# Kernel optimization log

Measured on AMD Instinct MI355X. Metric: run time of the kernel, lower is better.

## Reference

```python
import jax, jax.numpy as jnp
import numpy as np

BLUR_SIGMA = 5.0      # init kwarg blur_sigma
N_SIGMAS_PER_SIDE = 4 # fixed in module source
FLOW_AMP = 1.0        # init kwarg flow_amp
N_DIMS = 2            # len(img_shape) - 1


def _gaussian_kernel_2d(sigma, n_sigmas_per_side):
    # separable 2D gaussian spanning n_sigmas_per_side sigmas on each side, sum-normalized
    r = int(round(n_sigmas_per_side * sigma))
    x = np.arange(-r, r + 1, dtype=np.float32)
    g = np.exp(-(x ** 2) / (2.0 * sigma ** 2))
    k = np.outer(g, g)
    k /= k.sum()
    return jnp.asarray(k, dtype=jnp.float32)  # [kh, kw] = [41, 41] for sigma=5


def setup_inputs() -> dict:
    key = jax.random.key(0)
    k1, k2 = jax.random.split(key)
    inputs = jax.random.normal(k1, (16, 512, 512, 1), dtype=jnp.float32)
    # uniform in [0,1); scaled to [-flow_amp, flow_amp) inside reference
    rand_noise = jax.random.uniform(k2, (16, 512, 512, 2), dtype=jnp.float32)
    return {"inputs": inputs, "rand_noise": rand_noise}


def reference(inputs, rand_noise):
    # kernel tiled identically over the n_dims flow channels (depthwise, multiplier=1)
    k2d = _gaussian_kernel_2d(BLUR_SIGMA, N_SIGMAS_PER_SIDE)
    kernel = jnp.tile(k2d[:, :, None, None], (1, 1, 1, N_DIMS))  # HWIO: [41,41,1,2]
    # K.random_uniform(minval=-flow_amp, maxval=flow_amp)
    flow = rand_noise * (2.0 * FLOW_AMP) - FLOW_AMP  # [B,H,W,2]
    # tf.nn.depthwise_conv2d(..., strides=1, padding='SAME')
    out = jax.lax.conv_general_dilated(
        flow, kernel,
        window_strides=(1, 1),
        padding="SAME",
        dimension_numbers=("NHWC", "HWIO", "NHWC"),
        feature_group_count=N_DIMS,
    )  # [B,H,W,2] == reshape to (-1,)+flow_shape (no-op here)
    return out
```

## Files before the change

### kernel.cpp

```cpp
#include <hip/hip_runtime.h>

#define NB   16
#define H    512
#define W    512
#define KW   41
#define HALO 20

#define TX   88
#define TY   32
#define IN_W 128
#define PVV  16
#define PX   11
#define MSTR 129
#define OSTR 89
#define SMEM_F2 (TY * MSTR)

constexpr float G[KW] = {
  0.0003354626f, 0.0007318024f, 0.0015338104f, 0.0030887172f,
  0.0059760229f, 0.0111089965f, 0.0198410947f, 0.0340474548f,
  0.0561347628f, 0.0889216176f, 0.1353352832f, 0.1978986990f,
  0.2780373005f, 0.3753110988f, 0.4867522560f, 0.6065306597f,
  0.7261490371f, 0.8352702114f, 0.9231163464f, 0.9801986733f,
  1.0f,
  0.9801986733f, 0.9231163464f, 0.8352702114f, 0.7261490371f,
  0.6065306597f, 0.4867522560f, 0.3753110988f, 0.2780373005f,
  0.1978986990f, 0.1353352832f, 0.0889216176f, 0.0561347628f,
  0.0340474548f, 0.0198410947f, 0.0111089965f, 0.0059760229f,
  0.0030887172f, 0.0015338104f, 0.0007318024f, 0.0003354626f
};

constexpr float gsum() { float s = 0.f; for (int i = 0; i < KW; ++i) s += G[i]; return s; }
constexpr float INV_S2 = 1.0f / (gsum() * gsum());

__global__ __launch_bounds__(256, 4)
void randflow_blur_kernel(const float* __restrict__ noise, float* __restrict__ out) {
    __shared__ float2 smem[SMEM_F2];

    const int tid = threadIdx.x;
    const int bx  = blockIdx.x;
    const int tx0 = bx * TX;
    const int ty0 = blockIdx.y * TY;
    const int b   = blockIdx.z;
    const float* __restrict__ src = noise + (size_t)b * (H * W * 2);

    {
        const int sx  = tid & 127;
        const int yg  = tid >> 7;
        const int gx  = tx0 + sx - HALO;
        const int cgx = min(max(gx, 0), W - 1);
        const float sa = (gx == cgx) ? 2.0f : 0.0f;
        const float sb = (gx == cgx) ? -1.0f : 0.0f;
        const int  ysb = ty0 + yg * PVV - HALO;
        const float* __restrict__ colp = src + 2 * cgx;

        float2 acc[PVV];
        #pragma unroll
        for (int p = 0; p < PVV; ++p) acc[p] = make_float2(0.f, 0.f);

        #pragma unroll
        for (int j = 0; j < PVV + KW - 1; ++j) {
            const int ys = ysb + j;
            const int cy = min(max(ys, 0), H - 1);
            const float a  = (ys == cy) ? sa : 0.0f;
            const float bb = (ys == cy) ? sb : 0.0f;
            const float2 u = *(const float2*)(colp + (size_t)cy * (W * 2));
            float2 v;
            v.x = __builtin_fmaf(u.x, a, bb);
            v.y = __builtin_fmaf(u.y, a, bb);
            #pragma unroll
            for (int p = 0; p < PVV; ++p) {
                const int t = j - p;
                if (t >= 0 && t < KW) {
                    acc[p].x = __builtin_fmaf(G[t], v.x, acc[p].x);
                    acc[p].y = __builtin_fmaf(G[t], v.y, acc[p].y);
                }
            }
        }
        #pragma unroll
        for (int p = 0; p < PVV; ++p)
            smem[(yg * PVV + p) * MSTR + sx] = acc[p];
    }
    __syncthreads();

    const int y  = tid & 31;
    const int xg = tid >> 5;
    const int x0 = xg * PX;
    float2 facc[PX];
    {
        #pragma unroll
        for (int p = 0; p < PX; ++p) facc[p] = make_float2(0.f, 0.f);
        #pragma unroll
        for (int j = 0; j < PX + KW - 1; ++j) {
            const float2 v = smem[y * MSTR + x0 + j];
            #pragma unroll
            for (int p = 0; p < PX; ++p) {
                const int t = j - p;
                if (t >= 0 && t < KW) {
                    facc[p].x = __builtin_fmaf(G[t], v.x, facc[p].x);
                    facc[p].y = __builtin_fmaf(G[t], v.y, facc[p].y);
                }
            }
        }
    }
    __syncthreads();

    #pragma unroll
    for (int p = 0; p < PX; ++p) {
        float2 r;
        r.x = facc[p].x * INV_S2;
        r.y = facc[p].y * INV_S2;
        smem[y * OSTR + x0 + p] = r;
    }
    __syncthreads();

    #pragma unroll
    for (int p = 0; p < PX; ++p) {
        const int flat = p * 256 + tid;
        const int ry = flat / TX;
        const int rx = flat - ry * TX;
        const int xo = tx0 + rx;
        if (xo < W) {
            const int yo = ty0 + ry;
            *(float2*)(out + (((size_t)b * H + yo) * W + xo) * 2) = smem[ry * OSTR + rx];
        }
    }
}

extern "C" void kernel_launch(void* const* d_in, const int* in_sizes, int n_in,
                              void* d_out, int out_size, void* d_ws, size_t ws_size,
                              hipStream_t stream) {
    const float* noise = (const float*)d_in[1];
    float* out = (float*)d_out;

    dim3 grid((W + TX - 1) / TX, H / TY, NB);
    dim3 block(256);
    randflow_blur_kernel<<<grid, block, 0, stream>>>(noise, out);
}
```

Before: 124.2 us.

## Split blur into vertical and horizontal kernels with fp16 intermediate in workspace

Replaces the fused tile kernel with two passes when workspace is large enough. The first pass does the vertical 41-tap blur straight from global memory with no halo recompute in x and stores the result as half2. The second pass does the horizontal blur from an LDS tile with a padded layout and writes float4. The split removes the fused kernel's horizontal halo redundancy, at the cost of an extra global round trip through an fp16 buffer that loses precision. The original fused kernel is kept as a fallback.

```diff
diff --git a/kernel.cpp b/kernel.cpp
--- a/kernel.cpp
+++ b/kernel.cpp
@@ -1,4 +1,5 @@
 #include <hip/hip_runtime.h>
+#include <hip/hip_fp16.h>
 
 #define NB   16
 #define H    512
@@ -6,14 +7,14 @@
 #define KW   41
 #define HALO 20
 
-#define TX   88
-#define TY   32
-#define IN_W 128
-#define PVV  16
-#define PX   11
-#define MSTR 129
-#define OSTR 89
-#define SMEM_F2 (TY * MSTR)
+#define PVV  32
+
+#define ROWS 8
+#define TLOG 552
+#define TPHYS 825
+#define PX   16
+
+__device__ __forceinline__ int PHYS(int x) { return x + ((x >> 4) << 3); }
 
 constexpr float G[KW] = {
   0.0003354626f, 0.0007318024f, 0.0015338104f, 0.0030887172f,
@@ -28,21 +29,123 @@
   0.0340474548f, 0.0198410947f, 0.0111089965f, 0.0059760229f,
   0.0030887172f, 0.0015338104f, 0.0007318024f, 0.0003354626f
 };
-
 constexpr float gsum() { float s = 0.f; for (int i = 0; i < KW; ++i) s += G[i]; return s; }
+constexpr float INV_S  = 1.0f / gsum();
 constexpr float INV_S2 = 1.0f / (gsum() * gsum());
 
-__global__ __launch_bounds__(256, 4)
-void randflow_blur_kernel(const float* __restrict__ noise, float* __restrict__ out) {
-    __shared__ float2 smem[SMEM_F2];
-
+__global__ __launch_bounds__(256, 2)
+void kv_vertical(const float* __restrict__ noise, __half2* __restrict__ mid) {
     const int tid = threadIdx.x;
     const int bx  = blockIdx.x;
-    const int tx0 = bx * TX;
-    const int ty0 = blockIdx.y * TY;
+    const int b   = blockIdx.y;
+    const int x   = (bx & 1) * 256 + tid;
+    const int yg  = bx >> 1;
+    const int ysb = yg * PVV - HALO;
+    const float* __restrict__ colp = noise + ((size_t)b * (H * W) + x) * 2;
+
+    float2 acc[PVV];
+    #pragma unroll
+    for (int p = 0; p < PVV; ++p) acc[p] = make_float2(0.f, 0.f);
+
+    #pragma unroll
+    for (int j = 0; j < PVV + KW - 1; ++j) {
+        const int ys = ysb + j;
+        const int cy = min(max(ys, 0), H - 1);
+        const float a  = (ys == cy) ? 2.0f : 0.0f;
+        const float bb = (ys == cy) ? -1.0f : 0.0f;
+        const float2 u = *(const float2*)(colp + (size_t)cy * (W * 2));
+        float2 v;
+        v.x = __builtin_fmaf(u.x, a, bb);
+        v.y = __builtin_fmaf(u.y, a, bb);
+        #pragma unroll
+        for (int p = 0; p < PVV; ++p) {
+            const int t = j - p;
+            if (t >= 0 && t < KW) {
+                acc[p].x = __builtin_fmaf(G[t], v.x, acc[p].x);
+                acc[p].y = __builtin_fmaf(G[t], v.y, acc[p].y);
+            }
+        }
+    }
+    __half2* __restrict__ mb = mid + (size_t)b * (H * W) + x;
+    #pragma unroll
+    for (int p = 0; p < PVV; ++p) {
+        float2 r;
+        r.x = acc[p].x * INV_S;
+        r.y = acc[p].y * INV_S;
+        mb[(size_t)(yg * PVV + p) * W] = __float22half2_rn(r);
+    }
+}
+
+__global__ __launch_bounds__(256, 4)
+void kh_horizontal(const __half2* __restrict__ mid, float* __restrict__ out) {
+    __shared__ __half2 tile[ROWS * TPHYS];
+
+    const int tid = threadIdx.x;
+    const int rb  = blockIdx.x;
+    const int b   = blockIdx.y;
+    const int y0  = rb * ROWS;
+    const __half2* __restrict__ mb = mid + (size_t)b * (H * W) + (size_t)y0 * W;
+
+    for (int i = tid; i < ROWS * TLOG; i += 256) {
+        const int r  = i / TLOG;
+        const int cc = i - r * TLOG;
+        const int xs = cc - HALO;
+        __half2 v = __float2half2_rn(0.0f);
+        if ((unsigned)xs < (unsigned)W) v = mb[r * W + xs];
+        tile[r * TPHYS + PHYS(cc)] = v;
+    }
+    __syncthreads();
+
+    const int y  = tid & 7;
+    const int xg = tid >> 3;
+    const int x0 = xg * PX;
+    float2 acc[PX];
+    #pragma unroll
+    for (int p = 0; p < PX; ++p) acc[p] = make_float2(0.f, 0.f);
+
+    const __half2* __restrict__ trow = tile + y * TPHYS;
+    #pragma unroll
+    for (int j = 0; j < PX + KW - 1; ++j) {
+        const float2 v = __half22float2(trow[PHYS(x0 + j)]);
+        #pragma unroll
+        for (int p = 0; p < PX; ++p) {
+            const int t = j - p;
+            if (t >= 0 && t < KW) {
+                acc[p].x = __builtin_fmaf(G[t], v.x, acc[p].x);
+                acc[p].y = __builtin_fmaf(G[t], v.y, acc[p].y);
+            }
+        }
+    }
+
+    float2* __restrict__ orow = (float2*)out + ((size_t)b * H + y0 + y) * W;
+    #pragma unroll
+    for (int q = 0; q < PX / 2; ++q) {
+        float4 r;
+        r.x = acc[2*q].x   * INV_S;
+        r.y = acc[2*q].y   * INV_S;
+        r.z = acc[2*q+1].x * INV_S;
+        r.w = acc[2*q+1].y * INV_S;
+        *(float4*)&orow[x0 + 2*q] = r;
+    }
+}
+
+#define TXF   88
+#define TYF   32
+#define PVVF  16
+#define PXF   11
+#define MSTR  129
+#define OSTR  89
+#define SMEM_F2 (TYF * MSTR)
+
+__global__ __launch_bounds__(256, 4)
+void randflow_fused(const float* __restrict__ noise, float* __restrict__ out) {
+    __shared__ float2 smem[SMEM_F2];
+    const int tid = threadIdx.x;
+    const int bx  = blockIdx.x;
+    const int tx0 = bx * TXF;
+    const int ty0 = blockIdx.y * TYF;
     const int b   = blockIdx.z;
     const float* __restrict__ src = noise + (size_t)b * (H * W * 2);
-
     {
         const int sx  = tid & 127;
         const int yg  = tid >> 7;
@@ -50,15 +153,13 @@
         const int cgx = min(max(gx, 0), W - 1);
         const float sa = (gx == cgx) ? 2.0f : 0.0f;
         const float sb = (gx == cgx) ? -1.0f : 0.0f;
-        const int  ysb = ty0 + yg * PVV - HALO;
+        const int  ysb = ty0 + yg * PVVF - HALO;
         const float* __restrict__ colp = src + 2 * cgx;
-
-        float2 acc[PVV];
-        #pragma unroll
-        for (int p = 0; p < PVV; ++p) acc[p] = make_float2(0.f, 0.f);
-
-        #pragma unroll
-        for (int j = 0; j < PVV + KW - 1; ++j) {
+        float2 acc[PVVF];
+        #pragma unroll
+        for (int p = 0; p < PVVF; ++p) acc[p] = make_float2(0.f, 0.f);
+        #pragma unroll
+        for (int j = 0; j < PVVF + KW - 1; ++j) {
             const int ys = ysb + j;
             const int cy = min(max(ys, 0), H - 1);
             const float a  = (ys == cy) ? sa : 0.0f;
@@ -68,7 +169,7 @@
             v.x = __builtin_fmaf(u.x, a, bb);
             v.y = __builtin_fmaf(u.y, a, bb);
             #pragma unroll
-            for (int p = 0; p < PVV; ++p) {
+            for (int p = 0; p < PVVF; ++p) {
                 const int t = j - p;
                 if (t >= 0 && t < KW) {
                     acc[p].x = __builtin_fmaf(G[t], v.x, acc[p].x);
@@ -77,23 +178,22 @@
             }
         }
         #pragma unroll
-        for (int p = 0; p < PVV; ++p)
-            smem[(yg * PVV + p) * MSTR + sx] = acc[p];
-    }
-    __syncthreads();
-
+        for (int p = 0; p < PVVF; ++p)
+            smem[(yg * PVVF + p) * MSTR + sx] = acc[p];
+    }
+    __syncthreads();
     const int y  = tid & 31;
     const int xg = tid >> 5;
-    const int x0 = xg * PX;
-    float2 facc[PX];
+    const int x0 = xg * PXF;
+    float2 facc[PXF];
     {
         #pragma unroll
-        for (int p = 0; p < PX; ++p) facc[p] = make_float2(0.f, 0.f);
-        #pragma unroll
-        for (int j = 0; j < PX + KW - 1; ++j) {
+        for (int p = 0; p < PXF; ++p) facc[p] = make_float2(0.f, 0.f);
+        #pragma unroll
+        for (int j = 0; j < PXF + KW - 1; ++j) {
             const float2 v = smem[y * MSTR + x0 + j];
             #pragma unroll
-            for (int p = 0; p < PX; ++p) {
+            for (int p = 0; p < PXF; ++p) {
                 const int t = j - p;
                 if (t >= 0 && t < KW) {
                     facc[p].x = __builtin_fmaf(G[t], v.x, facc[p].x);
@@ -103,21 +203,19 @@
         }
     }
     __syncthreads();
-
-    #pragma unroll
-    for (int p = 0; p < PX; ++p) {
+    #pragma unroll
+    for (int p = 0; p < PXF; ++p) {
         float2 r;
         r.x = facc[p].x * INV_S2;
         r.y = facc[p].y * INV_S2;
         smem[y * OSTR + x0 + p] = r;
     }
     __syncthreads();
-
-    #pragma unroll
-    for (int p = 0; p < PX; ++p) {
+    #pragma unroll
+    for (int p = 0; p < PXF; ++p) {
         const int flat = p * 256 + tid;
-        const int ry = flat / TX;
-        const int rx = flat - ry * TX;
+        const int ry = flat / TXF;
+        const int rx = flat - ry * TXF;
         const int xo = tx0 + rx;
         if (xo < W) {
             const int yo = ty0 + ry;
@@ -132,7 +230,15 @@
     const float* noise = (const float*)d_in[1];
     float* out = (float*)d_out;
 
-    dim3 grid((W + TX - 1) / TX, H / TY, NB);
-    dim3 block(256);
-    randflow_blur_kernel<<<grid, block, 0, stream>>>(noise, out);
-}
+    const size_t mid_bytes = (size_t)NB * H * W * sizeof(__half2);
+    if (ws_size >= mid_bytes) {
+        __half2* mid = (__half2*)d_ws;
+        dim3 gv(32, NB);
+        kv_vertical<<<gv, dim3(256), 0, stream>>>(noise, mid);
+        dim3 gh(H / ROWS, NB);
+        kh_horizontal<<<gh, dim3(256), 0, stream>>>(mid, out);
+    } else {
+        dim3 gf((W + TXF - 1) / TXF, H / TYF, NB);
+        randflow_fused<<<gf, dim3(256), 0, stream>>>(noise, out);
+    }
+}
```

After: 175.7 us. 41.5% more time.
